# Optimization experiments

Measured on AMD Instinct MI355X. Metric: run time of the kernel, lower is better.

## Reference

```python
import jax, jax.numpy as jnp
import numpy as np

NEG_SLOPE = 0.01  # torch nn.LeakyReLU default
N_NODES, N_EDGES, N_BATCH, L_PATH = 100000, 300000, 50000, 4
D_EMB, D_HID, N_HEADS = 128, 64, 8


def setup_inputs() -> dict:
    key = jax.random.key(0)
    ks = jax.random.split(key, 10)
    return {
        "batch_nodes": jax.random.randint(ks[0], (N_BATCH,), 0, N_NODES),
        "metapath_indices": jax.random.randint(ks[1], (N_EDGES, L_PATH), 0, N_NODES),
        "edge_dst": jax.random.randint(ks[2], (N_EDGES,), 0, N_NODES),
        "transformed_feature": jax.random.normal(ks[3], (N_NODES, D_EMB), jnp.float32),
        "W_i": jax.random.normal(ks[4], (D_HID, D_EMB), jnp.float32) * 0.05,
        "W_p": jax.random.normal(ks[5], (D_HID, D_EMB), jnp.float32) * 0.05,
        "attn": jax.random.normal(ks[6], (1, N_HEADS, D_HID), jnp.float32) * 0.05,
        "W_th": jax.random.normal(ks[7], (N_HEADS, N_HEADS), jnp.float32) * 0.3,
        "W_gate": jax.random.normal(ks[8], (1, D_HID), jnp.float32) * 0.1,
        "b_gate": jnp.zeros((1,), jnp.float32),
    }


def reference(batch_nodes, metapath_indices, edge_dst, transformed_feature,
              W_i, W_p, attn, W_th, W_gate, b_gate):
    N = transformed_feature.shape[0]
    # node_type_specific_agg for mtype==1: h_src/h_dst through linear_i, h_p1/h_p2 through linear_p
    membd = transformed_feature[metapath_indices]                      # [E, 4, D_emb]
    edata = (membd[:, 0] + membd[:, 3]) @ W_i.T \
          + (membd[:, 1] + membd[:, 2]) @ W_p.T                        # [E, D]
    E, D = edata.shape
    H = attn.shape[1]
    # cat([edata]*H, dim=1).view(-1, H, D) duplicates edata per head
    efeat = jnp.broadcast_to(edata[:, None, :], (E, H, D))             # [E, H, D]
    # talking-heads attention logits, leaky-relu
    logits = (efeat * attn).sum(-1) @ W_th.T                           # [E, H]
    logits = jax.nn.leaky_relu(logits, NEG_SLOPE)
    # dgl edge_softmax: per-dst-node, per-head softmax over incoming edges (stable)
    m = jax.ops.segment_max(logits, edge_dst, num_segments=N)          # [N, H]
    ex = jnp.exp(logits - m[edge_dst])                                 # [E, H]
    den = jax.ops.segment_sum(ex, edge_dst, num_segments=N)            # [N, H]
    a = ex / den[edge_dst]                                             # [E, H]  (dropout rate 0)
    # message passing: ft = efeature * a, summed per dst node
    msgs = (efeat * a[:, :, None]).reshape(E, H * D)
    node_ft = jax.ops.segment_sum(msgs, edge_dst, num_segments=N)      # [N, H*D]
    result = node_ft[batch_nodes].reshape(-1, H, D)                    # [B, H, D]
    # gated multi-head attention: gate = mean over batch of fc_gate(result)
    gate = jnp.mean(result @ W_gate.T + b_gate, axis=0)                # [H, 1]
    result = result * gate[None]                                       # [B, H, D]
    return result.reshape(-1, H * D)
```

## Files before the change

### kernel.cpp

```cpp
#include <hip/hip_runtime.h>
#include <cstdint>
#include <cstddef>


typedef __attribute__((ext_vector_type(8))) short bf16x8;
typedef __attribute__((ext_vector_type(4))) float f32x4;
typedef __attribute__((ext_vector_type(8))) unsigned short u16x8;

__device__ __forceinline__ unsigned short f2bf(float f) {
    unsigned u = __float_as_uint(f);
    unsigned r = u + 0x7fffu + ((u >> 16) & 1u);
    return (unsigned short)(r >> 16);
}
__device__ __forceinline__ float bf2f(unsigned short h) {
    return __uint_as_float((unsigned)h << 16);
}
__device__ __forceinline__ unsigned fenc(float f) {
    unsigned u = __float_as_uint(f);
    return (u & 0x80000000u) ? ~u : (u | 0x80000000u);
}
__device__ __forceinline__ float fdec(unsigned k) {
    unsigned u = (k & 0x80000000u) ? (k & 0x7fffffffu) : ~k;
    return __uint_as_float(u);
}

__global__ __launch_bounds__(256) void k_prep(
    const float* __restrict__ Wi, const float* __restrict__ Wp,
    unsigned short* __restrict__ Whi, unsigned short* __restrict__ Wlo,
    const int* __restrict__ batch_nodes, int* __restrict__ mult, int B) {
    int t = blockIdx.x * 256 + threadIdx.x;
    if (t < B) atomicAdd(&mult[batch_nodes[t]], 1);
    if (t >= 16384) return;
    int j = t & 7, L = (t >> 3) & 63, c = (t >> 9) & 7, s = t >> 12;
    int k = s * 32 + (L >> 4) * 8 + j;
    int n = c * 16 + (L & 15);
    float v = (n < 64) ? Wi[n * 128 + k] : Wp[(n - 64) * 128 + k];
    unsigned short h = f2bf(v);
    Whi[t] = h;
    Wlo[t] = f2bf(v - bf2f(h));
}

__global__ __launch_bounds__(256) void k_dense(
    const float* __restrict__ feat, const unsigned short* __restrict__ Whi,
    const unsigned short* __restrict__ Wlo, const float* __restrict__ attn,
    const int* __restrict__ edge_dst, const int* __restrict__ mult,
    int* __restrict__ count, unsigned short* __restrict__ Ybf,
    float* __restrict__ P, int M, int E) {
    int t = threadIdx.x;

    {
        int e = blockIdx.x * 256 + t;
        if (e < E) {
            int d = edge_dst[e];
            if (mult[d] > 0) atomicAdd(&count[d], 1);
        }
    }

    int L = t & 63;
    int wave = t >> 6;
    int m = L & 15, q = L >> 4;
    int R0 = blockIdx.x * 64 + wave * 16;

    int rowc = R0 + m; if (rowc > M - 1) rowc = M - 1;
    const float* arow = feat + (size_t)rowc * 128;

    float4 av0[4], av1[4];
#pragma unroll
    for (int s = 0; s < 4; ++s) {
        const float4* ap = (const float4*)(arow + s * 32 + q * 8);
        av0[s] = ap[0];
        av1[s] = ap[1];
    }
    bf16x8 ahi[4], alo[4];
#pragma unroll
    for (int s = 0; s < 4; ++s) {
        float av[8] = {av0[s].x, av0[s].y, av0[s].z, av0[s].w,
                       av1[s].x, av1[s].y, av1[s].z, av1[s].w};
#pragma unroll
        for (int j = 0; j < 8; ++j) {
            unsigned short h = f2bf(av[j]);
            ahi[s][j] = (short)h;
            alo[s][j] = (short)f2bf(av[j] - bf2f(h));
        }
    }

    f32x4 acc[8];
#pragma unroll
    for (int c = 0; c < 8; ++c) acc[c] = (f32x4){0.f, 0.f, 0.f, 0.f};

    const bf16x8* gh = (const bf16x8*)Whi;
    const bf16x8* gl = (const bf16x8*)Wlo;
#pragma unroll
    for (int s = 0; s < 4; ++s) {
#pragma unroll
        for (int c = 0; c < 8; ++c) {
            bf16x8 bh = gh[(s * 8 + c) * 64 + L];
            bf16x8 bl = gl[(s * 8 + c) * 64 + L];
            acc[c] = __builtin_amdgcn_mfma_f32_16x16x32_bf16(ahi[s], bh, acc[c], 0, 0, 0);
            acc[c] = __builtin_amdgcn_mfma_f32_16x16x32_bf16(ahi[s], bl, acc[c], 0, 0, 0);
            acc[c] = __builtin_amdgcn_mfma_f32_16x16x32_bf16(alo[s], bh, acc[c], 0, 0, 0);
        }
    }

#pragma unroll
    for (int c = 0; c < 8; ++c) {
#pragma unroll
        for (int r = 0; r < 4; ++r) {
            int row = R0 + q * 4 + r;
            if (row < M) Ybf[(size_t)row * 128 + c * 16 + m] = f2bf(acc[c][r]);
        }
    }
#pragma unroll
    for (int i = 0; i < 8; ++i) {
        float a0 = attn[i * 64 + m];
        float a1 = attn[i * 64 + 16 + m];
        float a2 = attn[i * 64 + 32 + m];
        float a3 = attn[i * 64 + 48 + m];
#pragma unroll
        for (int r = 0; r < 4; ++r) {
            int row = R0 + q * 4 + r;
            float pi = acc[0][r] * a0 + acc[1][r] * a1 + acc[2][r] * a2 + acc[3][r] * a3;
            float pp = acc[4][r] * a0 + acc[5][r] * a1 + acc[6][r] * a2 + acc[7][r] * a3;
#pragma unroll
            for (int o = 1; o < 16; o <<= 1) {
                pi += __shfl_xor(pi, o);
                pp += __shfl_xor(pp, o);
            }
            if (row < M) {
                if (m == i)     P[(size_t)row * 16 + i] = pi;
                if (m == i + 8) P[(size_t)row * 16 + 8 + i] = pp;
            }
        }
    }
}

__global__ __launch_bounds__(256) void k_scan1(
    const int* __restrict__ count, int* __restrict__ excl, int* __restrict__ partials, int N) {
    __shared__ int lds[256];
    int t = threadIdx.x, i = blockIdx.x * 256 + t;
    int c = (i < N) ? count[i] : 0;
    lds[t] = c; __syncthreads();
    for (int o = 1; o < 256; o <<= 1) {
        int v = (t >= o) ? lds[t - o] : 0;
        __syncthreads(); lds[t] += v; __syncthreads();
    }
    if (i < N) excl[i] = lds[t] - c;
    if (t == 255) partials[blockIdx.x] = lds[255];
}

__global__ __launch_bounds__(256) void k_scan23(
    const int* __restrict__ excl, const int* __restrict__ partials,
    int* __restrict__ offsets, int* __restrict__ cursor, int N) {
    __shared__ int sacc[256];
    int bid = blockIdx.x, t = threadIdx.x;
    int s = 0;
    for (int j = t; j < bid; j += 256) s += partials[j];
    sacc[t] = s; __syncthreads();
#pragma unroll
    for (int o = 128; o > 0; o >>= 1) {
        if (t < o) sacc[t] += sacc[t + o];
        __syncthreads();
    }
    int boff = sacc[0];
    int i = bid * 256 + t;
    if (i < N) {
        int o = excl[i] + boff;
        offsets[i] = o; cursor[i] = o;
    }
    if (t == 0 && bid == gridDim.x - 1) offsets[N] = boff + partials[bid];
}

__global__ __launch_bounds__(256) void k_scatter_logits(
    const int* __restrict__ edge_dst, const int* __restrict__ mult,
    int* __restrict__ cursor, const int* __restrict__ mp,
    const float* __restrict__ P, const float* __restrict__ Wth,
    float* __restrict__ logits, int4* __restrict__ mpc,
    unsigned* __restrict__ mxkey, int E) {
    int e = blockIdx.x * 32 + (threadIdx.x >> 3);
    if (e >= E) return;
    int h = threadIdx.x & 7;
    int d = edge_dst[e];
    if (mult[d] == 0) return;
    int pos = 0;
    if (h == 0) pos = atomicAdd(&cursor[d], 1);
    int gbase = threadIdx.x & ~7;
    pos = __shfl(pos, gbase);
    int4 rows = *(const int4*)(mp + (size_t)e * 4);
    float s = P[(size_t)rows.x * 16 + h] + P[(size_t)rows.w * 16 + h]
            + P[(size_t)rows.y * 16 + 8 + h] + P[(size_t)rows.z * 16 + 8 + h];
    float l = 0.f;
#pragma unroll
    for (int j = 0; j < 8; ++j) {
        float sj = __shfl(s, gbase + j);
        l += Wth[h * 8 + j] * sj;
    }
    l = l > 0.f ? l : 0.01f * l;
    logits[(size_t)pos * 8 + h] = l;
    atomicMax(&mxkey[(size_t)d * 8 + h], fenc(l));
    if (h == 0) mpc[pos] = rows;
}

__global__ __launch_bounds__(256) void k_node_agg(
    const unsigned short* __restrict__ Ybf, const float* __restrict__ logits,
    const int4* __restrict__ mpc, const int* __restrict__ offsets,
    const int* __restrict__ mult, const unsigned* __restrict__ mxkey,
    const float* __restrict__ Wg,
    unsigned short* __restrict__ nftb, float* __restrict__ gate_part, int N) {
    int n = blockIdx.x * 4 + (threadIdx.x >> 6);
    int lane = threadIdx.x & 63;
    if (n >= N) return;
    int m = mult[n];
    if (m == 0) return;
    int beg = offsets[n], end = offsets[n + 1];

    float mx[8], den[8], acc[8];
#pragma unroll
    for (int h = 0; h < 8; ++h) {
        mx[h] = fdec(mxkey[(size_t)n * 8 + h]);
        den[h] = 0.f; acc[h] = 0.f;
    }

    for (int j = beg; j < end; ++j) {
        const float4* lp = (const float4*)(logits + (size_t)j * 8);
        float4 l0 = lp[0], l1 = lp[1];
        int4 rows = mpc[j];
        float ed = bf2f(Ybf[(size_t)rows.x * 128 + lane])
                 + bf2f(Ybf[(size_t)rows.w * 128 + lane])
                 + bf2f(Ybf[(size_t)rows.y * 128 + 64 + lane])
                 + bf2f(Ybf[(size_t)rows.z * 128 + 64 + lane]);
        float w0 = __expf(l0.x - mx[0]), w1 = __expf(l0.y - mx[1]);
        float w2 = __expf(l0.z - mx[2]), w3 = __expf(l0.w - mx[3]);
        float w4 = __expf(l1.x - mx[4]), w5 = __expf(l1.y - mx[5]);
        float w6 = __expf(l1.z - mx[6]), w7 = __expf(l1.w - mx[7]);
        den[0] += w0; den[1] += w1; den[2] += w2; den[3] += w3;
        den[4] += w4; den[5] += w5; den[6] += w6; den[7] += w7;
        acc[0] += w0 * ed; acc[1] += w1 * ed; acc[2] += w2 * ed; acc[3] += w3 * ed;
        acc[4] += w4 * ed; acc[5] += w5 * ed; acc[6] += w6 * ed; acc[7] += w7 * ed;
    }

#pragma unroll
    for (int h = 0; h < 8; ++h) {
        float r = (end > beg) ? 1.f / den[h] : 0.f;
        acc[h] *= r;
    }

    unsigned short* base = nftb + (size_t)n * 512;
#pragma unroll
    for (int h = 0; h < 8; ++h) base[h * 64 + lane] = f2bf(acc[h]);

    float wg = Wg[lane];
    float myg = 0.f;
#pragma unroll
    for (int h = 0; h < 8; ++h) {
        float p = acc[h] * wg;
#pragma unroll
        for (int o = 32; o > 0; o >>= 1) p += __shfl_xor(p, o);
        if (lane == h) myg = p;
    }
    if (lane < 8)
        atomicAdd(&gate_part[(blockIdx.x & 1023) * 8 + lane], (float)m * myg);
}

__global__ __launch_bounds__(256) void k_gatefinal(
    const float* __restrict__ gate_part, const float* __restrict__ b_gate,
    float* __restrict__ gate, int B) {
    __shared__ float lds[256];
    int t = threadIdx.x;
    int h = t & 7, g = t >> 3;
    float s = 0.f;
    for (int b = g; b < 1024; b += 32) s += gate_part[b * 8 + h];
    lds[t] = s; __syncthreads();
    if (t < 8) {
        float tot = 0.f;
        for (int gg = 0; gg < 32; ++gg) tot += lds[gg * 8 + t];
        gate[t] = tot / (float)B + b_gate[0];
    }
}

__global__ __launch_bounds__(256) void k_output(
    const unsigned short* __restrict__ nftb, const int* __restrict__ batch_nodes,
    const float* __restrict__ gate, float* __restrict__ out, int B) {
    int idx = blockIdx.x * 256 + threadIdx.x;
    int total = B * 64;
    if (idx >= total) return;
    int b = idx >> 6;
    int r = idx & 63;
    int h = r >> 3;
    int n = batch_nodes[b];
    u16x8 v = *(const u16x8*)(nftb + (size_t)n * 512 + r * 8);
    float g = gate[h];
    f32x4 o0, o1;
    o0[0] = bf2f(v[0]) * g; o0[1] = bf2f(v[1]) * g;
    o0[2] = bf2f(v[2]) * g; o0[3] = bf2f(v[3]) * g;
    o1[0] = bf2f(v[4]) * g; o1[1] = bf2f(v[5]) * g;
    o1[2] = bf2f(v[6]) * g; o1[3] = bf2f(v[7]) * g;
    f32x4* op = (f32x4*)(out + (size_t)idx * 8);
    __builtin_nontemporal_store(o0, op);
    __builtin_nontemporal_store(o1, op + 1);
}

extern "C" void kernel_launch(void* const* d_in, const int* in_sizes, int n_in,
                              void* d_out, int out_size, void* d_ws, size_t ws_size,
                              hipStream_t stream) {
    const int*   batch_nodes = (const int*)d_in[0];
    const int*   mp          = (const int*)d_in[1];
    const int*   edge_dst    = (const int*)d_in[2];
    const float* feat        = (const float*)d_in[3];
    const float* W_i         = (const float*)d_in[4];
    const float* W_p         = (const float*)d_in[5];
    const float* attn        = (const float*)d_in[6];
    const float* W_th        = (const float*)d_in[7];
    const float* W_gate      = (const float*)d_in[8];
    const float* b_gate      = (const float*)d_in[9];
    float* out = (float*)d_out;

    const int B = in_sizes[0];
    const int E = in_sizes[2];
    const int N = in_sizes[3] / 128;
    const int nb_scan = (N + 255) / 256;

    char* w = (char*)d_ws;
    auto alloc = [&](size_t bytes) -> void* {
        void* p = (void*)w;
        w += (bytes + 255) & ~(size_t)255;
        return p;
    };
    unsigned short* Whi = (unsigned short*)alloc(16384 * 2);
    unsigned short* Wlo = (unsigned short*)alloc(16384 * 2);
    unsigned short* Ybf = (unsigned short*)alloc((size_t)N * 128 * 2);
    float* P            = (float*)alloc((size_t)N * 16 * 4);
    float* logits       = (float*)alloc((size_t)E * 8 * 4);
    int4*  mpc          = (int4*)alloc((size_t)E * 16);
    size_t zero_bytes   = (size_t)N * 4 + (size_t)N * 4 + 1024 * 8 * 4
                        + (size_t)N * 8 * 4;
    int*   mult         = (int*)alloc(zero_bytes);
    int*   count        = mult + N;
    float* gate_part    = (float*)(count + N);
    unsigned* mxkey     = (unsigned*)(gate_part + 8192);
    int*   excl         = (int*)alloc((size_t)N * 4);
    int*   offsets      = (int*)alloc((size_t)(N + 1) * 4);
    int*   cursor       = (int*)alloc((size_t)N * 4);
    int*   partials     = (int*)alloc(512 * 4);
    unsigned short* nftb = (unsigned short*)alloc((size_t)N * 512 * 2);
    float* gate         = (float*)alloc(256);

    hipMemsetAsync(mult, 0, zero_bytes, stream);

    int prep_work = (B > 16384) ? B : 16384;
    k_prep<<<(prep_work + 255) / 256, 256, 0, stream>>>(W_i, W_p, Whi, Wlo,
                                                        batch_nodes, mult, B);
    k_dense<<<(N + 63) / 64, 256, 0, stream>>>(feat, Whi, Wlo, attn,
                                               edge_dst, mult, count, Ybf, P, N, E);
    k_scan1<<<nb_scan, 256, 0, stream>>>(count, excl, partials, N);
    k_scan23<<<nb_scan, 256, 0, stream>>>(excl, partials, offsets, cursor, N);
    k_scatter_logits<<<(E + 31) / 32, 256, 0, stream>>>(edge_dst, mult, cursor,
                                                        mp, P, W_th, logits, mpc,
                                                        mxkey, E);
    k_node_agg<<<(N + 3) / 4, 256, 0, stream>>>(Ybf, logits, mpc, offsets, mult,
                                                mxkey, W_gate, nftb, gate_part, N);
    k_gatefinal<<<1, 256, 0, stream>>>(gate_part, b_gate, gate, B);
    k_output<<<(B * 64 + 255) / 256, 256, 0, stream>>>(nftb, batch_nodes, gate, out, B);
}
```

Baseline: 315.0 us.

## Fuse scan passes with decoupled lookback and fold gate reduction into output

The two-kernel prefix scan becomes a single kernel. Each block publishes its total with a flag and then spins on the flags of earlier blocks, which removes a launch and the intermediate excl/partials buffers. The single-block gate finalisation now runs redundantly at the start of each output block, and the output kernel becomes a grid-stride loop over 2048 blocks. k_dense also gets a min-blocks hint of 4 per CU. The cost is spin-waiting in the scan, which relies on forward progress of earlier-indexed blocks, and every output block repeats the 8K-float gate reduction.

```diff
diff --git a/kernel.cpp b/kernel.cpp
--- a/kernel.cpp
+++ b/kernel.cpp
@@ -40,7 +40,7 @@
     Wlo[t] = f2bf(v - bf2f(h));
 }
 
-__global__ __launch_bounds__(256) void k_dense(
+__global__ __launch_bounds__(256, 4) void k_dense(
     const float* __restrict__ feat, const unsigned short* __restrict__ Whi,
     const unsigned short* __restrict__ Wlo, const float* __restrict__ attn,
     const int* __restrict__ edge_dst, const int* __restrict__ mult,
@@ -134,40 +134,47 @@
     }
 }
 
-__global__ __launch_bounds__(256) void k_scan1(
-    const int* __restrict__ count, int* __restrict__ excl, int* __restrict__ partials, int N) {
+#define SCAN_FLAG 0x40000000u
+__global__ __launch_bounds__(256) void k_scan(
+    const int* __restrict__ count, int* __restrict__ offsets,
+    int* __restrict__ cursor, unsigned* __restrict__ state, int N) {
     __shared__ int lds[256];
-    int t = threadIdx.x, i = blockIdx.x * 256 + t;
+    int bid = blockIdx.x, t = threadIdx.x;
+    int i = bid * 256 + t;
     int c = (i < N) ? count[i] : 0;
     lds[t] = c; __syncthreads();
     for (int o = 1; o < 256; o <<= 1) {
         int v = (t >= o) ? lds[t - o] : 0;
         __syncthreads(); lds[t] += v; __syncthreads();
     }
-    if (i < N) excl[i] = lds[t] - c;
-    if (t == 255) partials[blockIdx.x] = lds[255];
-}
-
-__global__ __launch_bounds__(256) void k_scan23(
-    const int* __restrict__ excl, const int* __restrict__ partials,
-    int* __restrict__ offsets, int* __restrict__ cursor, int N) {
-    __shared__ int sacc[256];
-    int bid = blockIdx.x, t = threadIdx.x;
+    int incl = lds[t];
+    int total = lds[255];
+    int excl = incl - c;
+    if (t == 0)
+        __hip_atomic_store(&state[(size_t)bid * 16], (unsigned)total | SCAN_FLAG,
+                           __ATOMIC_RELEASE, __HIP_MEMORY_SCOPE_AGENT);
     int s = 0;
-    for (int j = t; j < bid; j += 256) s += partials[j];
-    sacc[t] = s; __syncthreads();
+    for (int j = t; j < bid; j += 256) {
+        unsigned v;
+        do {
+            v = __hip_atomic_load(&state[(size_t)j * 16], __ATOMIC_ACQUIRE,
+                                  __HIP_MEMORY_SCOPE_AGENT);
+        } while (!(v & SCAN_FLAG));
+        s += (int)(v & (SCAN_FLAG - 1u));
+    }
+    __syncthreads();
+    lds[t] = s; __syncthreads();
 #pragma unroll
     for (int o = 128; o > 0; o >>= 1) {
-        if (t < o) sacc[t] += sacc[t + o];
+        if (t < o) lds[t] += lds[t + o];
         __syncthreads();
     }
-    int boff = sacc[0];
-    int i = bid * 256 + t;
+    int boff = lds[0];
     if (i < N) {
-        int o = excl[i] + boff;
-        offsets[i] = o; cursor[i] = o;
-    }
-    if (t == 0 && bid == gridDim.x - 1) offsets[N] = boff + partials[bid];
+        int off = boff + excl;
+        offsets[i] = off; cursor[i] = off;
+    }
+    if (t == 255 && bid == gridDim.x - 1) offsets[N] = boff + total;
 }
 
 __global__ __launch_bounds__(256) void k_scatter_logits(
@@ -261,42 +268,43 @@
         atomicAdd(&gate_part[(blockIdx.x & 1023) * 8 + lane], (float)m * myg);
 }
 
-__global__ __launch_bounds__(256) void k_gatefinal(
-    const float* __restrict__ gate_part, const float* __restrict__ b_gate,
-    float* __restrict__ gate, int B) {
-    __shared__ float lds[256];
-    int t = threadIdx.x;
-    int h = t & 7, g = t >> 3;
-    float s = 0.f;
-    for (int b = g; b < 1024; b += 32) s += gate_part[b * 8 + h];
-    lds[t] = s; __syncthreads();
-    if (t < 8) {
-        float tot = 0.f;
-        for (int gg = 0; gg < 32; ++gg) tot += lds[gg * 8 + t];
-        gate[t] = tot / (float)B + b_gate[0];
-    }
-}
-
 __global__ __launch_bounds__(256) void k_output(
     const unsigned short* __restrict__ nftb, const int* __restrict__ batch_nodes,
-    const float* __restrict__ gate, float* __restrict__ out, int B) {
-    int idx = blockIdx.x * 256 + threadIdx.x;
+    const float* __restrict__ gate_part, const float* __restrict__ b_gate,
+    float* __restrict__ out, int B) {
+    __shared__ float lds[256];
+    __shared__ float sg[8];
+    int t = threadIdx.x;
+    {
+        int h = t & 7, g = t >> 3;
+        float s = 0.f;
+        for (int b = g; b < 1024; b += 32) s += gate_part[b * 8 + h];
+        lds[t] = s; __syncthreads();
+        if (t < 8) {
+            float tot = 0.f;
+            for (int gg = 0; gg < 32; ++gg) tot += lds[gg * 8 + t];
+            sg[t] = tot / (float)B + b_gate[0];
+        }
+        __syncthreads();
+    }
     int total = B * 64;
-    if (idx >= total) return;
-    int b = idx >> 6;
-    int r = idx & 63;
-    int h = r >> 3;
-    int n = batch_nodes[b];
-    u16x8 v = *(const u16x8*)(nftb + (size_t)n * 512 + r * 8);
-    float g = gate[h];
-    f32x4 o0, o1;
-    o0[0] = bf2f(v[0]) * g; o0[1] = bf2f(v[1]) * g;
-    o0[2] = bf2f(v[2]) * g; o0[3] = bf2f(v[3]) * g;
-    o1[0] = bf2f(v[4]) * g; o1[1] = bf2f(v[5]) * g;
-    o1[2] = bf2f(v[6]) * g; o1[3] = bf2f(v[7]) * g;
-    f32x4* op = (f32x4*)(out + (size_t)idx * 8);
-    __builtin_nontemporal_store(o0, op);
-    __builtin_nontemporal_store(o1, op + 1);
+    int stride = gridDim.x * 256;
+    for (int idx = blockIdx.x * 256 + t; idx < total; idx += stride) {
+        int b = idx >> 6;
+        int r = idx & 63;
+        int h = r >> 3;
+        int n = batch_nodes[b];
+        u16x8 v = *(const u16x8*)(nftb + (size_t)n * 512 + r * 8);
+        float g = sg[h];
+        f32x4 o0, o1;
+        o0[0] = bf2f(v[0]) * g; o0[1] = bf2f(v[1]) * g;
+        o0[2] = bf2f(v[2]) * g; o0[3] = bf2f(v[3]) * g;
+        o1[0] = bf2f(v[4]) * g; o1[1] = bf2f(v[5]) * g;
+        o1[2] = bf2f(v[6]) * g; o1[3] = bf2f(v[7]) * g;
+        f32x4* op = (f32x4*)(out + (size_t)idx * 8);
+        __builtin_nontemporal_store(o0, op);
+        __builtin_nontemporal_store(o1, op + 1);
+    }
 }
 
 extern "C" void kernel_launch(void* const* d_in, const int* in_sizes, int n_in,
@@ -331,33 +339,30 @@
     float* P            = (float*)alloc((size_t)N * 16 * 4);
     float* logits       = (float*)alloc((size_t)E * 8 * 4);
     int4*  mpc          = (int4*)alloc((size_t)E * 16);
-    size_t zero_bytes   = (size_t)N * 4 + (size_t)N * 4 + 1024 * 8 * 4
-                        + (size_t)N * 8 * 4;
-    int*   mult         = (int*)alloc(zero_bytes);
+    size_t zero_ints    = (size_t)N + (size_t)N + 8192 + (size_t)N * 8 + 512 * 16;
+    int*   mult         = (int*)alloc(zero_ints * 4);
     int*   count        = mult + N;
     float* gate_part    = (float*)(count + N);
     unsigned* mxkey     = (unsigned*)(gate_part + 8192);
-    int*   excl         = (int*)alloc((size_t)N * 4);
+    unsigned* sstate    = mxkey + (size_t)N * 8;
     int*   offsets      = (int*)alloc((size_t)(N + 1) * 4);
     int*   cursor       = (int*)alloc((size_t)N * 4);
-    int*   partials     = (int*)alloc(512 * 4);
     unsigned short* nftb = (unsigned short*)alloc((size_t)N * 512 * 2);
     float* gate         = (float*)alloc(256);
-
-    hipMemsetAsync(mult, 0, zero_bytes, stream);
+    (void)gate;
+
+    hipMemsetAsync(mult, 0, zero_ints * 4, stream);
 
     int prep_work = (B > 16384) ? B : 16384;
     k_prep<<<(prep_work + 255) / 256, 256, 0, stream>>>(W_i, W_p, Whi, Wlo,
                                                         batch_nodes, mult, B);
     k_dense<<<(N + 63) / 64, 256, 0, stream>>>(feat, Whi, Wlo, attn,
                                                edge_dst, mult, count, Ybf, P, N, E);
-    k_scan1<<<nb_scan, 256, 0, stream>>>(count, excl, partials, N);
-    k_scan23<<<nb_scan, 256, 0, stream>>>(excl, partials, offsets, cursor, N);
+    k_scan<<<nb_scan, 256, 0, stream>>>(count, offsets, cursor, sstate, N);
     k_scatter_logits<<<(E + 31) / 32, 256, 0, stream>>>(edge_dst, mult, cursor,
                                                         mp, P, W_th, logits, mpc,
                                                         mxkey, E);
     k_node_agg<<<(N + 3) / 4, 256, 0, stream>>>(Ybf, logits, mpc, offsets, mult,
                                                 mxkey, W_gate, nftb, gate_part, N);
-    k_gatefinal<<<1, 256, 0, stream>>>(gate_part, b_gate, gate, B);
-    k_output<<<(B * 64 + 255) / 256, 256, 0, stream>>>(nftb, batch_nodes, gate, out, B);
-}
+    k_output<<<2048, 256, 0, stream>>>(nftb, batch_nodes, gate_part, b_gate, out, B);
+}
```

Result: slower. 331.3 us (+5.2%).
